# Optimization experiments

Measured on AMD Instinct MI355X. Metric: run time of the kernel, lower is better.

The kernel has to match this reference:

```python
import jax, jax.numpy as jnp
import numpy as np

B, G = 256, 4096
N_GENES, D_GENE = 30000, 256
D_HIDDEN, D_Z = 256, 64
EPS = 1e-8


def setup_inputs() -> dict:
    key = jax.random.key(0)
    ks = jax.random.split(key, 12)
    d_in = D_GENE + 1  # + log-libsize
    s = lambda fan_in: 1.0 / np.sqrt(fan_in)
    return {
        "x": jax.random.uniform(ks[0], (B, G), jnp.float32) * 5.0,  # expression counts
        "gene_indices": jax.random.randint(ks[1], (B, G), 0, N_GENES),
        "emb_table": jax.random.normal(ks[2], (N_GENES, D_GENE), jnp.float32) * 0.02,
        "W1": jax.random.normal(ks[3], (d_in, D_HIDDEN), jnp.float32) * s(d_in),
        "b1": jnp.zeros((D_HIDDEN,), jnp.float32),
        "W2": jax.random.normal(ks[4], (D_HIDDEN, D_HIDDEN), jnp.float32) * s(D_HIDDEN),
        "b2": jnp.zeros((D_HIDDEN,), jnp.float32),
        "Wmu": jax.random.normal(ks[5], (D_HIDDEN, D_Z), jnp.float32) * s(D_HIDDEN),
        "bmu": jnp.zeros((D_Z,), jnp.float32),
        "Wlv": jax.random.normal(ks[6], (D_HIDDEN, D_Z), jnp.float32) * s(D_HIDDEN),
        "blv": jnp.zeros((D_Z,), jnp.float32),
    }


def reference(x, gene_indices, emb_table, W1, b1, W2, b2, Wmu, bmu, Wlv, blv):
    # pool_genes: gather (B,G,d) then weighted-sum reduce to (B,d)
    gene_embs = emb_table[gene_indices]                      # (B, G, d)
    w = jnp.log1p(x)
    w = w / (w.sum(axis=1, keepdims=True) + EPS)             # (B, G)
    h_pool = jnp.einsum('bg,bgd->bd', w, gene_embs)          # (B, d)

    log_lib = jnp.log1p(x.sum(axis=1))[:, None]              # (B, 1)
    h = jnp.concatenate([h_pool, log_lib], axis=-1)          # (B, d+1)

    h = jax.nn.relu(h @ W1 + b1)                             # dropout: eval-mode identity
    h = jax.nn.relu(h @ W2 + b2)
    mu_z = h @ Wmu + bmu
    logvar_z = h @ Wlv + blv
    return (mu_z, logvar_z, h_pool)
```

## Files before the change

kernel.cpp:

```cpp
#include <hip/hip_runtime.h>
#include <math.h>

#define BB      256
#define GG      4096
#define DG      256
#define DH      256
#define DZ      64
#define NGENES  30000
#define KPAD    30016
#define NCHUNK  (KPAD / 32)
#define KSPLIT  128
#define RED     16
#define NPART2  (KSPLIT / RED)
#define HALF    (KPAD / 2)
#define FB_TILES (NCHUNK * 16)
#define SPLIT   4
#define GCHUNK  (GG / SPLIT)

typedef __attribute__((ext_vector_type(8))) short  short8v;
typedef __attribute__((ext_vector_type(4))) float  floatx4;

__device__ __forceinline__ unsigned short bf16_rn(float f) {
    unsigned u = __float_as_uint(f);
    u += 0x7FFFu + ((u >> 16) & 1u);
    return (unsigned short)(u >> 16);
}

__global__ __launch_bounds__(256) void scatter_kernel(
    const float* __restrict__ x,
    const int*   __restrict__ gi,
    unsigned short* __restrict__ W16,
    float* __restrict__ wsum,
    float* __restrict__ xsum)
{
    const int b   = blockIdx.x;
    const int h   = blockIdx.y;
    const int tid = threadIdx.x;
    const int base = h * HALF;

    __shared__ float sW[HALF];
    for (int i = tid; i < HALF; i += 256) sW[i] = 0.f;
    __syncthreads();

    const float4* x4 = (const float4*)(x  + (size_t)b * GG);
    const int4*   g4 = (const int4*)  (gi + (size_t)b * GG);

    float lws = 0.f, xs = 0.f;
    #pragma unroll
    for (int it = 0; it < 4; ++it) {
        const int    e  = it * 256 + tid;
        const float4 xv = x4[e];
        const int4   iv = g4[e];
        const float lw0 = log1pf(xv.x), lw1 = log1pf(xv.y);
        const float lw2 = log1pf(xv.z), lw3 = log1pf(xv.w);
        lws += lw0 + lw1 + lw2 + lw3;
        xs  += xv.x + xv.y + xv.z + xv.w;
        int r0 = iv.x - base, r1 = iv.y - base, r2 = iv.z - base, r3 = iv.w - base;
        if ((unsigned)r0 < (unsigned)HALF) atomicAdd(&sW[r0], lw0);
        if ((unsigned)r1 < (unsigned)HALF) atomicAdd(&sW[r1], lw1);
        if ((unsigned)r2 < (unsigned)HALF) atomicAdd(&sW[r2], lw2);
        if ((unsigned)r3 < (unsigned)HALF) atomicAdd(&sW[r3], lw3);
    }
    __syncthreads();

    uint4* dst = (uint4*)(W16 + (size_t)b * KPAD + base);
    for (int i = tid; i < HALF / 8; i += 256) {
        const float* s = &sW[i * 8];
        uint4 o;
        o.x = (unsigned)bf16_rn(s[0]) | ((unsigned)bf16_rn(s[1]) << 16);
        o.y = (unsigned)bf16_rn(s[2]) | ((unsigned)bf16_rn(s[3]) << 16);
        o.z = (unsigned)bf16_rn(s[4]) | ((unsigned)bf16_rn(s[5]) << 16);
        o.w = (unsigned)bf16_rn(s[6]) | ((unsigned)bf16_rn(s[7]) << 16);
        dst[i] = o;
    }
    __syncthreads();

    #pragma unroll
    for (int off = 32; off > 0; off >>= 1) {
        lws += __shfl_down(lws, off);
        xs  += __shfl_down(xs,  off);
    }
    if ((tid & 63) == 0) { sW[tid >> 6] = lws; sW[4 + (tid >> 6)] = xs; }
    __syncthreads();
    if (tid == 0 && h == 0) {
        wsum[b] = sW[0] + sW[1] + sW[2] + sW[3];
        xsum[b] = sW[4] + sW[5] + sW[6] + sW[7];
    }
}

__global__ __launch_bounds__(256) void fragb_kernel(
    const float* __restrict__ emb, unsigned short* __restrict__ fragB)
{
    const int tile = blockIdx.x * 4 + (threadIdx.x >> 6);
    const int lane = threadIdx.x & 63;
    const int kc = tile >> 4;
    const int nt = tile & 15;
    const int n  = (nt << 4) + (lane & 15);
    const int k0 = (kc << 5) + ((lane >> 4) << 3);

    unsigned short v[8] __attribute__((aligned(16)));
    #pragma unroll
    for (int j = 0; j < 8; ++j) {
        const int k = k0 + j;
        v[j] = (k < NGENES) ? bf16_rn(emb[(size_t)k * DG + n]) : (unsigned short)0;
    }
    *(uint4*)(fragB + (size_t)tile * 512 + lane * 8) = *(const uint4*)v;
}

__global__ __launch_bounds__(256) void gemm_kernel(
    const unsigned short* __restrict__ W16,
    const unsigned short* __restrict__ fragB,
    float* __restrict__ ws_gemm)
{
    const int mt   = blockIdx.x;
    const int ks   = blockIdx.y;
    const int tid  = threadIdx.x;
    const int w    = tid >> 6;
    const int lane = tid & 63;
    const int quad = lane >> 4;
    const int l16  = lane & 15;

    const int q = NCHUNK / KSPLIT;
    const int r = NCHUNK % KSPLIT;
    const int c0  = (ks < r) ? ks * (q + 1) : r * (q + 1) + (ks - r) * q;
    const int cnt = (ks < r) ? (q + 1) : q;

    __shared__ short8v sB[1024];

    const unsigned short* Arow =
        W16 + (size_t)((mt << 6) + (w << 4) + l16) * KPAD + (quad << 3);

    floatx4 acc[16];
    #pragma unroll
    for (int nt = 0; nt < 16; ++nt) acc[nt] = (floatx4){0.f, 0.f, 0.f, 0.f};

    for (int c = 0; c < cnt; ++c) {
        const int kc = c0 + c;

        const short8v af = *(const short8v*)(Arow + (kc << 5));

        const uint4* src = (const uint4*)(fragB + (size_t)kc * 8192);
        #pragma unroll
        for (int i = 0; i < 4; ++i)
            ((uint4*)sB)[i * 256 + tid] = src[i * 256 + tid];

        __syncthreads();
        #pragma unroll
        for (int nt = 0; nt < 16; ++nt) {
            const short8v bf = sB[nt * 64 + lane];
            acc[nt] = __builtin_amdgcn_mfma_f32_16x16x32_bf16(af, bf, acc[nt], 0, 0, 0);
        }
        __syncthreads();
    }

    #pragma unroll
    for (int nt = 0; nt < 16; ++nt) {
        #pragma unroll
        for (int reg = 0; reg < 4; ++reg) {
            const int m = (mt << 6) + (w << 4) + (quad << 2) + reg;
            const int n = (nt << 4) + l16;
            ws_gemm[((size_t)m * KSPLIT + ks) * DG + n] = acc[nt][reg];
        }
    }
}

__global__ __launch_bounds__(256) void reduce_kernel(
    const float* __restrict__ wsg, float* __restrict__ part2)
{
    const int b = blockIdx.x, p = blockIdx.y, d = threadIdx.x;
    const float* src = wsg + ((size_t)b * KSPLIT + p * RED) * DG + d;
    float s = 0.f;
    #pragma unroll
    for (int i = 0; i < RED; ++i) s += src[(size_t)i * DG];
    part2[((size_t)b * NPART2 + p) * DG + d] = s;
}

__global__ __launch_bounds__(256) void convert_kernel(
    const float* __restrict__ emb, unsigned short* __restrict__ embh, int n4)
{
    const float4* e4 = (const float4*)emb;
    ushort4*      o4 = (ushort4*)embh;
    const int stride = gridDim.x * 256;
    for (int i = blockIdx.x * 256 + threadIdx.x; i < n4; i += stride) {
        const float4 v = e4[i];
        ushort4 o;
        o.x = bf16_rn(v.x); o.y = bf16_rn(v.y);
        o.z = bf16_rn(v.z); o.w = bf16_rn(v.w);
        o4[i] = o;
    }
}

__global__ __launch_bounds__(256) void pool_bf16_kernel(
    const float*          __restrict__ x,
    const int*            __restrict__ gi,
    const unsigned short* __restrict__ embh,
    float* __restrict__ ws_pool,
    float* __restrict__ ws_wsum,
    float* __restrict__ ws_xsum)
{
    const int b    = blockIdx.x;
    const int s    = blockIdx.y;
    const int tid  = threadIdx.x;
    const int wave = tid >> 6;
    const int lane = tid & 63;

    const float* xrow = x  + (size_t)b * GG + (size_t)s * GCHUNK;
    const int*   irow = gi + (size_t)b * GG + (size_t)s * GCHUNK;
    const uint2* emb2 = (const uint2*)embh;

    __shared__ float lw_s[256];
    __shared__ int   idx_s[256];
    __shared__ float accred[4][256];
    __shared__ float redw[4], redx[4];

    float wsum = 0.f, xsum = 0.f;
    float4 acc = make_float4(0.f, 0.f, 0.f, 0.f);

    for (int g0 = 0; g0 < GCHUNK; g0 += 256) {
        __syncthreads();
        const float xv = xrow[g0 + tid];
        const int   iv = irow[g0 + tid];
        const float lw = log1pf(xv);
        xsum += xv;
        wsum += lw;
        lw_s[tid]  = lw;
        idx_s[tid] = iv;
        __syncthreads();

        #pragma unroll 8
        for (int k = 0; k < 64; ++k) {
            const int   gidx = (k << 2) | wave;
            const float lw_b = lw_s[gidx];
            const uint2 e    = emb2[(size_t)idx_s[gidx] * 64 + lane];
            acc.x = fmaf(lw_b, __uint_as_float(e.x << 16),         acc.x);
            acc.y = fmaf(lw_b, __uint_as_float(e.x & 0xFFFF0000u), acc.y);
            acc.z = fmaf(lw_b, __uint_as_float(e.y << 16),         acc.z);
            acc.w = fmaf(lw_b, __uint_as_float(e.y & 0xFFFF0000u), acc.w);
        }
    }

    accred[wave][lane * 4 + 0] = acc.x;
    accred[wave][lane * 4 + 1] = acc.y;
    accred[wave][lane * 4 + 2] = acc.z;
    accred[wave][lane * 4 + 3] = acc.w;

    #pragma unroll
    for (int off = 32; off > 0; off >>= 1) {
        wsum += __shfl_down(wsum, off);
        xsum += __shfl_down(xsum, off);
    }
    if (lane == 0) { redw[wave] = wsum; redx[wave] = xsum; }
    __syncthreads();

    const float tot = accred[0][tid] + accred[1][tid] + accred[2][tid] + accred[3][tid];
    ws_pool[((size_t)b * SPLIT + s) * DG + tid] = tot;
    if (tid == 0) {
        ws_wsum[b * SPLIT + s] = redw[0] + redw[1] + redw[2] + redw[3];
        ws_xsum[b * SPLIT + s] = redx[0] + redx[1] + redx[2] + redx[3];
    }
}

template <int NS, int NW>
__global__ __launch_bounds__(512) void mlp_kernel(
    const float* __restrict__ part,
    const float* __restrict__ wsA, const float* __restrict__ xsA,
    const float* __restrict__ W1, const float* __restrict__ b1,
    const float* __restrict__ W2, const float* __restrict__ b2,
    const float* __restrict__ Wmu, const float* __restrict__ bmu,
    const float* __restrict__ Wlv, const float* __restrict__ blv,
    float* __restrict__ out)
{
    const int b   = blockIdx.x;
    const int tid = threadIdx.x;
    const int kq  = tid >> 6;
    const int c4  = tid & 63;

    __shared__ float  h[DH + 1];
    __shared__ float  h1[DH];
    __shared__ float  h2[DH];
    __shared__ float4 red[8][64];
    __shared__ float  redz[8][64];

    if (tid < DH) {
        float acc = 0.f;
        #pragma unroll
        for (int s = 0; s < NS; ++s)
            acc += part[((size_t)b * NS + s) * DG + tid];
        float wsum = 0.f, xsum = 0.f;
        #pragma unroll
        for (int s = 0; s < NW; ++s) {
            wsum += wsA[b * NW + s];
            xsum += xsA[b * NW + s];
        }
        const float hp = acc / (wsum + 1e-8f);
        out[2 * BB * DZ + (size_t)b * DG + tid] = hp;
        h[tid] = hp;
        if (tid == 0) h[DH] = log1pf(xsum);
    }
    __syncthreads();

    {
        const float4* Wv = (const float4*)W1;
        float4 a = make_float4(0.f, 0.f, 0.f, 0.f);
        const int i0 = kq * 32;
        const int i1 = i0 + 32 + (kq == 7 ? 1 : 0);
        for (int i = i0; i < i1; ++i) {
            const float  hi = h[i];
            const float4 w  = Wv[(size_t)i * 64 + c4];
            a.x = fmaf(hi, w.x, a.x);
            a.y = fmaf(hi, w.y, a.y);
            a.z = fmaf(hi, w.z, a.z);
            a.w = fmaf(hi, w.w, a.w);
        }
        red[kq][c4] = a;
        __syncthreads();
        if (tid < 64) {
            float4 t = red[0][tid];
            #pragma unroll
            for (int s = 1; s < 8; ++s) {
                const float4 rr = red[s][tid];
                t.x += rr.x; t.y += rr.y; t.z += rr.z; t.w += rr.w;
            }
            const float4 bb = ((const float4*)b1)[tid];
            h1[4 * tid + 0] = fmaxf(t.x + bb.x, 0.f);
            h1[4 * tid + 1] = fmaxf(t.y + bb.y, 0.f);
            h1[4 * tid + 2] = fmaxf(t.z + bb.z, 0.f);
            h1[4 * tid + 3] = fmaxf(t.w + bb.w, 0.f);
        }
        __syncthreads();
    }

    {
        const float4* Wv = (const float4*)W2;
        float4 a = make_float4(0.f, 0.f, 0.f, 0.f);
        const int i0 = kq * 32;
        for (int i = i0; i < i0 + 32; ++i) {
            const float  hi = h1[i];
            const float4 w  = Wv[(size_t)i * 64 + c4];
            a.x = fmaf(hi, w.x, a.x);
            a.y = fmaf(hi, w.y, a.y);
            a.z = fmaf(hi, w.z, a.z);
            a.w = fmaf(hi, w.w, a.w);
        }
        red[kq][c4] = a;
        __syncthreads();
        if (tid < 64) {
            float4 t = red[0][tid];
            #pragma unroll
            for (int s = 1; s < 8; ++s) {
                const float4 rr = red[s][tid];
                t.x += rr.x; t.y += rr.y; t.z += rr.z; t.w += rr.w;
            }
            const float4 bb = ((const float4*)b2)[tid];
            h2[4 * tid + 0] = fmaxf(t.x + bb.x, 0.f);
            h2[4 * tid + 1] = fmaxf(t.y + bb.y, 0.f);
            h2[4 * tid + 2] = fmaxf(t.z + bb.z, 0.f);
            h2[4 * tid + 3] = fmaxf(t.w + bb.w, 0.f);
        }
        __syncthreads();
    }

    {
        const bool is_lv = tid >= 256;
        const int  j  = tid & 63;
        const int  kh = (tid >> 6) & 3;
        const float* Wz = is_lv ? Wlv : Wmu;
        float az = 0.f;
        for (int i = kh * 64; i < kh * 64 + 64; ++i)
            az = fmaf(h2[i], Wz[(size_t)i * DZ + j], az);
        redz[(is_lv ? 4 : 0) + kh][j] = az;
        __syncthreads();
        if (tid < 2 * DZ) {
            const bool lv = tid >= DZ;
            const int  jj = tid & (DZ - 1);
            const int  base = lv ? 4 : 0;
            float rr = redz[base][jj] + redz[base + 1][jj]
                     + redz[base + 2][jj] + redz[base + 3][jj];
            rr += lv ? blv[jj] : bmu[jj];
            out[(lv ? BB * DZ : 0) + (size_t)b * DZ + jj] = rr;
        }
    }
}

extern "C" void kernel_launch(void* const* d_in, const int* in_sizes, int n_in,
                              void* d_out, int out_size, void* d_ws, size_t ws_size,
                              hipStream_t stream) {
    const float* x    = (const float*)d_in[0];
    const int*   gi   = (const int*)  d_in[1];
    const float* emb  = (const float*)d_in[2];
    const float* W1   = (const float*)d_in[3];
    const float* b1   = (const float*)d_in[4];
    const float* W2   = (const float*)d_in[5];
    const float* b2   = (const float*)d_in[6];
    const float* Wmu  = (const float*)d_in[7];
    const float* bmu  = (const float*)d_in[8];
    const float* Wlv  = (const float*)d_in[9];
    const float* blv  = (const float*)d_in[10];
    float* out = (float*)d_out;

    char* ws = (char*)d_ws;
    float* ws_wsum = (float*)(ws + 0);
    float* ws_xsum = (float*)(ws + 4096);
    const size_t off_main = 8192;

    const size_t szW   = (size_t)BB * KPAD * sizeof(unsigned short);
    const size_t szFB  = (size_t)FB_TILES * 1024;
    const size_t szGP  = (size_t)BB * KSPLIT * DG * sizeof(float);
    const size_t szP2  = (size_t)BB * NPART2 * DG * sizeof(float);
    const size_t need_full = off_main + szW + szFB + szGP + szP2;

    const size_t szPool = (size_t)BB * SPLIT * DG * sizeof(float);
    const size_t szEmbh = (size_t)NGENES * DG * sizeof(unsigned short);
    const size_t need_fb = off_main + szPool + szEmbh;

    if (ws_size >= need_full) {
        unsigned short* Wm    = (unsigned short*)(ws + off_main);
        unsigned short* fragB = (unsigned short*)(ws + off_main + szW);
        float*          wsg   = (float*)(ws + off_main + szW + szFB);
        float*          part2 = (float*)(ws + off_main + szW + szFB + szGP);

        scatter_kernel<<<dim3(BB, 2), 256, 0, stream>>>(x, gi, Wm, ws_wsum, ws_xsum);
        fragb_kernel<<<FB_TILES / 4, 256, 0, stream>>>(emb, fragB);
        gemm_kernel<<<dim3(4, KSPLIT), 256, 0, stream>>>(Wm, fragB, wsg);
        reduce_kernel<<<dim3(BB, NPART2), 256, 0, stream>>>(wsg, part2);
        mlp_kernel<NPART2, 1><<<BB, 512, 0, stream>>>(part2, ws_wsum, ws_xsum,
                                           W1, b1, W2, b2, Wmu, bmu, Wlv, blv, out);
    } else if (ws_size >= need_fb) {
        float*          ws_pool = (float*)(ws + off_main);
        unsigned short* embh    = (unsigned short*)(ws + off_main + szPool);

        convert_kernel<<<2048, 256, 0, stream>>>(emb, embh, NGENES * DG / 4);
        pool_bf16_kernel<<<dim3(BB, SPLIT), 256, 0, stream>>>(
            x, gi, embh, ws_pool, ws_wsum, ws_xsum);
        mlp_kernel<SPLIT, SPLIT><<<BB, 512, 0, stream>>>(ws_pool, ws_wsum, ws_xsum,
                                           W1, b1, W2, b2, Wmu, bmu, Wlv, blv, out);
    }
}
```

Measured before the change: 143.1 us.

## Double-buffer GEMM B tiles and store split-K partials as bf16

The GEMM kernel now prefetches the next K-chunk of B fragments and A into registers while running MFMAs on the current chunk, with a two-slot shared buffer and one barrier per iteration instead of two. The split-K partial sums are rounded to bf16, staged through shared memory, and written as coalesced 16-byte stores, halving the partial-sum workspace traffic. The reduce kernel reads the bf16 partials. This targets load latency and write/read bandwidth of the partial buffer, at the cost of extra precision loss in the split-K partials and more shared memory per block.

Measured after the change: 149.6 us. 4.6% more time.

```diff
diff --git a/kernel.cpp b/kernel.cpp
--- a/kernel.cpp
+++ b/kernel.cpp
@@ -110,7 +110,7 @@
 __global__ __launch_bounds__(256) void gemm_kernel(
     const unsigned short* __restrict__ W16,
     const unsigned short* __restrict__ fragB,
-    float* __restrict__ ws_gemm)
+    unsigned short* __restrict__ wsg16)
 {
     const int mt   = blockIdx.x;
     const int ks   = blockIdx.y;
@@ -122,10 +122,10 @@
 
     const int q = NCHUNK / KSPLIT;
     const int r = NCHUNK % KSPLIT;
-    const int c0  = (ks < r) ? ks * (q + 1) : r * (q + 1) + (ks - r) * q;
-    const int cnt = (ks < r) ? (q + 1) : q;
-
-    __shared__ short8v sB[1024];
+    const int c0  = ks * q + (ks < r ? ks : r);
+    const int cnt = q + (ks < r ? 1 : 0);
+
+    __shared__ short8v sB[2][1024];
 
     const unsigned short* Arow =
         W16 + (size_t)((mt << 6) + (w << 4) + l16) * KPAD + (quad << 3);
@@ -134,44 +134,67 @@
     #pragma unroll
     for (int nt = 0; nt < 16; ++nt) acc[nt] = (floatx4){0.f, 0.f, 0.f, 0.f};
 
+    uint4 breg[4];
+    {
+        const uint4* src = (const uint4*)(fragB + (size_t)c0 * 8192);
+        #pragma unroll
+        for (int i = 0; i < 4; ++i) breg[i] = src[i * 256 + tid];
+    }
+    short8v af = *(const short8v*)(Arow + ((size_t)c0 << 5));
+    #pragma unroll
+    for (int i = 0; i < 4; ++i) ((uint4*)sB[0])[i * 256 + tid] = breg[i];
+    __syncthreads();
+
     for (int c = 0; c < cnt; ++c) {
-        const int kc = c0 + c;
-
-        const short8v af = *(const short8v*)(Arow + (kc << 5));
-
-        const uint4* src = (const uint4*)(fragB + (size_t)kc * 8192);
-        #pragma unroll
-        for (int i = 0; i < 4; ++i)
-            ((uint4*)sB)[i * 256 + tid] = src[i * 256 + tid];
-
-        __syncthreads();
+        const int cur = c & 1;
+        short8v afn;
+        if (c + 1 < cnt) {
+            const uint4* src = (const uint4*)(fragB + (size_t)(c0 + c + 1) * 8192);
+            #pragma unroll
+            for (int i = 0; i < 4; ++i) breg[i] = src[i * 256 + tid];
+            afn = *(const short8v*)(Arow + ((size_t)(c0 + c + 1) << 5));
+        }
         #pragma unroll
         for (int nt = 0; nt < 16; ++nt) {
-            const short8v bf = sB[nt * 64 + lane];
+            const short8v bf = sB[cur][nt * 64 + lane];
             acc[nt] = __builtin_amdgcn_mfma_f32_16x16x32_bf16(af, bf, acc[nt], 0, 0, 0);
         }
-        __syncthreads();
-    }
-
+        if (c + 1 < cnt) {
+            #pragma unroll
+            for (int i = 0; i < 4; ++i) ((uint4*)sB[cur ^ 1])[i * 256 + tid] = breg[i];
+            af = afn;
+        }
+        __syncthreads();
+    }
+
+    unsigned short* epi = (unsigned short*)sB + (w << 12);
     #pragma unroll
     for (int nt = 0; nt < 16; ++nt) {
         #pragma unroll
-        for (int reg = 0; reg < 4; ++reg) {
-            const int m = (mt << 6) + (w << 4) + (quad << 2) + reg;
-            const int n = (nt << 4) + l16;
-            ws_gemm[((size_t)m * KSPLIT + ks) * DG + n] = acc[nt][reg];
-        }
+        for (int reg = 0; reg < 4; ++reg)
+            epi[((quad << 2) + reg) * 256 + (nt << 4) + l16] = bf16_rn(acc[nt][reg]);
+    }
+    uint4* wrow = (uint4*)wsg16;
+    #pragma unroll
+    for (int j = 0; j < 8; ++j) {
+        const int flat = lane + (j << 6);
+        const int rr   = flat >> 5;
+        const int u    = flat & 31;
+        const uint4 v  = *(const uint4*)(epi + rr * 256 + (u << 3));
+        const int m    = (mt << 6) + (w << 4) + rr;
+        wrow[(((size_t)m * KSPLIT + ks) << 5) + u] = v;
     }
 }
 
 __global__ __launch_bounds__(256) void reduce_kernel(
-    const float* __restrict__ wsg, float* __restrict__ part2)
+    const unsigned short* __restrict__ wsg16, float* __restrict__ part2)
 {
     const int b = blockIdx.x, p = blockIdx.y, d = threadIdx.x;
-    const float* src = wsg + ((size_t)b * KSPLIT + p * RED) * DG + d;
+    const unsigned short* src = wsg16 + ((size_t)b * KSPLIT + p * RED) * DG + d;
     float s = 0.f;
     #pragma unroll
-    for (int i = 0; i < RED; ++i) s += src[(size_t)i * DG];
+    for (int i = 0; i < RED; ++i)
+        s += __uint_as_float((unsigned)src[(size_t)i * DG] << 16);
     part2[((size_t)b * NPART2 + p) * DG + d] = s;
 }
 
@@ -405,7 +428,7 @@
 
     const size_t szW   = (size_t)BB * KPAD * sizeof(unsigned short);
     const size_t szFB  = (size_t)FB_TILES * 1024;
-    const size_t szGP  = (size_t)BB * KSPLIT * DG * sizeof(float);
+    const size_t szGP  = (size_t)BB * KSPLIT * DG * sizeof(unsigned short);
     const size_t szP2  = (size_t)BB * NPART2 * DG * sizeof(float);
     const size_t need_full = off_main + szW + szFB + szGP + szP2;
 
@@ -416,13 +439,13 @@
     if (ws_size >= need_full) {
         unsigned short* Wm    = (unsigned short*)(ws + off_main);
         unsigned short* fragB = (unsigned short*)(ws + off_main + szW);
-        float*          wsg   = (float*)(ws + off_main + szW + szFB);
+        unsigned short* wsg16 = (unsigned short*)(ws + off_main + szW + szFB);
         float*          part2 = (float*)(ws + off_main + szW + szFB + szGP);
 
         scatter_kernel<<<dim3(BB, 2), 256, 0, stream>>>(x, gi, Wm, ws_wsum, ws_xsum);
         fragb_kernel<<<FB_TILES / 4, 256, 0, stream>>>(emb, fragB);
-        gemm_kernel<<<dim3(4, KSPLIT), 256, 0, stream>>>(Wm, fragB, wsg);
-        reduce_kernel<<<dim3(BB, NPART2), 256, 0, stream>>>(wsg, part2);
+        gemm_kernel<<<dim3(4, KSPLIT), 256, 0, stream>>>(Wm, fragB, wsg16);
+        reduce_kernel<<<dim3(BB, NPART2), 256, 0, stream>>>(wsg16, part2);
         mlp_kernel<NPART2, 1><<<BB, 512, 0, stream>>>(part2, ws_wsum, ws_xsum,
                                            W1, b1, W2, b2, Wmu, bmu, Wlv, blv, out);
     } else if (ws_size >= need_fb) {
```

## Transpose embeddings via LDS, store split-K partials as bf16, remap gemm blocks

Applied to the files above, without the earlier changes.

fragb_kernel now loads a 32-row chunk of the embedding table with coalesced float4 reads into padded shared memory, then builds the bf16 MFMA B-fragments from LDS. Previously each lane did strided scalar global reads. The gemm kernel writes its split-K partial sums as bf16 instead of fp32, which halves the write and reread traffic through reduce_kernel. It also uses a 1D grid remapped so that blocks sharing the same K-chunk of fragB run close together, which should improve L2 reuse. Rounding the partials to bf16 adds precision loss to the pooled output.

Result: faster. 135.8 us (-5.1%).

```diff
diff --git a/kernel.cpp b/kernel.cpp
--- a/kernel.cpp
+++ b/kernel.cpp
@@ -14,6 +14,7 @@
 #define NPART2  (KSPLIT / RED)
 #define HALF    (KPAD / 2)
 #define FB_TILES (NCHUNK * 16)
+#define TSTRIDE 258
 #define SPLIT   4
 #define GCHUNK  (GG / SPLIT)
 
@@ -91,39 +92,59 @@
 __global__ __launch_bounds__(256) void fragb_kernel(
     const float* __restrict__ emb, unsigned short* __restrict__ fragB)
 {
-    const int tile = blockIdx.x * 4 + (threadIdx.x >> 6);
-    const int lane = threadIdx.x & 63;
-    const int kc = tile >> 4;
-    const int nt = tile & 15;
-    const int n  = (nt << 4) + (lane & 15);
-    const int k0 = (kc << 5) + ((lane >> 4) << 3);
-
-    unsigned short v[8] __attribute__((aligned(16)));
-    #pragma unroll
-    for (int j = 0; j < 8; ++j) {
-        const int k = k0 + j;
-        v[j] = (k < NGENES) ? bf16_rn(emb[(size_t)k * DG + n]) : (unsigned short)0;
-    }
-    *(uint4*)(fragB + (size_t)tile * 512 + lane * 8) = *(const uint4*)v;
-}
-
-__global__ __launch_bounds__(256) void gemm_kernel(
-    const unsigned short* __restrict__ W16,
-    const unsigned short* __restrict__ fragB,
-    float* __restrict__ ws_gemm)
-{
-    const int mt   = blockIdx.x;
-    const int ks   = blockIdx.y;
+    const int kc   = blockIdx.x;
     const int tid  = threadIdx.x;
     const int w    = tid >> 6;
     const int lane = tid & 63;
     const int quad = lane >> 4;
     const int l16  = lane & 15;
+    const int k0   = kc << 5;
+
+    __shared__ float sT[32 * TSTRIDE];
+
+    const float4* e4 = (const float4*)emb;
+    #pragma unroll
+    for (int i = 0; i < 8; ++i) {
+        const int f   = i * 256 + tid;
+        const int row = f >> 6;
+        const int col = f & 63;
+        float4 v = make_float4(0.f, 0.f, 0.f, 0.f);
+        if (k0 + row < NGENES) v = e4[(size_t)(k0 + row) * 64 + col];
+        float* d = &sT[row * TSTRIDE + (col << 2)];
+        *(float2*)d       = make_float2(v.x, v.y);
+        *(float2*)(d + 2) = make_float2(v.z, v.w);
+    }
+    __syncthreads();
+
+    #pragma unroll
+    for (int t = 0; t < 4; ++t) {
+        const int nt = (w << 2) + t;
+        unsigned short v[8] __attribute__((aligned(16)));
+        #pragma unroll
+        for (int j = 0; j < 8; ++j)
+            v[j] = bf16_rn(sT[(quad * 8 + j) * TSTRIDE + (nt << 4) + l16]);
+        *(uint4*)(fragB + (size_t)kc * 8192 + (nt << 9) + lane * 8) = *(const uint4*)v;
+    }
+}
+
+__global__ __launch_bounds__(256) void gemm_kernel(
+    const unsigned short* __restrict__ W16,
+    const unsigned short* __restrict__ fragB,
+    unsigned short* __restrict__ wsg16)
+{
+    const int bid  = blockIdx.x;
+    const int mt   = (bid >> 3) & 3;
+    const int ks   = ((bid >> 5) << 3) | (bid & 7);
+    const int tid  = threadIdx.x;
+    const int w    = tid >> 6;
+    const int lane = tid & 63;
+    const int quad = lane >> 4;
+    const int l16  = lane & 15;
 
     const int q = NCHUNK / KSPLIT;
     const int r = NCHUNK % KSPLIT;
-    const int c0  = (ks < r) ? ks * (q + 1) : r * (q + 1) + (ks - r) * q;
-    const int cnt = (ks < r) ? (q + 1) : q;
+    const int c0  = ks * q + (ks < r ? ks : r);
+    const int cnt = q + (ks < r ? 1 : 0);
 
     __shared__ short8v sB[1024];
 
@@ -137,7 +158,7 @@
     for (int c = 0; c < cnt; ++c) {
         const int kc = c0 + c;
 
-        const short8v af = *(const short8v*)(Arow + (kc << 5));
+        const short8v af = *(const short8v*)(Arow + ((size_t)kc << 5));
 
         const uint4* src = (const uint4*)(fragB + (size_t)kc * 8192);
         #pragma unroll
@@ -159,19 +180,20 @@
         for (int reg = 0; reg < 4; ++reg) {
             const int m = (mt << 6) + (w << 4) + (quad << 2) + reg;
             const int n = (nt << 4) + l16;
-            ws_gemm[((size_t)m * KSPLIT + ks) * DG + n] = acc[nt][reg];
+            wsg16[((size_t)m * KSPLIT + ks) * DG + n] = bf16_rn(acc[nt][reg]);
         }
     }
 }
 
 __global__ __launch_bounds__(256) void reduce_kernel(
-    const float* __restrict__ wsg, float* __restrict__ part2)
+    const unsigned short* __restrict__ wsg16, float* __restrict__ part2)
 {
     const int b = blockIdx.x, p = blockIdx.y, d = threadIdx.x;
-    const float* src = wsg + ((size_t)b * KSPLIT + p * RED) * DG + d;
+    const unsigned short* src = wsg16 + ((size_t)b * KSPLIT + p * RED) * DG + d;
     float s = 0.f;
     #pragma unroll
-    for (int i = 0; i < RED; ++i) s += src[(size_t)i * DG];
+    for (int i = 0; i < RED; ++i)
+        s += __uint_as_float((unsigned)src[(size_t)i * DG] << 16);
     part2[((size_t)b * NPART2 + p) * DG + d] = s;
 }
 
@@ -405,7 +427,7 @@
 
     const size_t szW   = (size_t)BB * KPAD * sizeof(unsigned short);
     const size_t szFB  = (size_t)FB_TILES * 1024;
-    const size_t szGP  = (size_t)BB * KSPLIT * DG * sizeof(float);
+    const size_t szGP  = (size_t)BB * KSPLIT * DG * sizeof(unsigned short);
     const size_t szP2  = (size_t)BB * NPART2 * DG * sizeof(float);
     const size_t need_full = off_main + szW + szFB + szGP + szP2;
 
@@ -416,13 +438,13 @@
     if (ws_size >= need_full) {
         unsigned short* Wm    = (unsigned short*)(ws + off_main);
         unsigned short* fragB = (unsigned short*)(ws + off_main + szW);
-        float*          wsg   = (float*)(ws + off_main + szW + szFB);
+        unsigned short* wsg16 = (unsigned short*)(ws + off_main + szW + szFB);
         float*          part2 = (float*)(ws + off_main + szW + szFB + szGP);
 
         scatter_kernel<<<dim3(BB, 2), 256, 0, stream>>>(x, gi, Wm, ws_wsum, ws_xsum);
-        fragb_kernel<<<FB_TILES / 4, 256, 0, stream>>>(emb, fragB);
-        gemm_kernel<<<dim3(4, KSPLIT), 256, 0, stream>>>(Wm, fragB, wsg);
-        reduce_kernel<<<dim3(BB, NPART2), 256, 0, stream>>>(wsg, part2);
+        fragb_kernel<<<NCHUNK, 256, 0, stream>>>(emb, fragB);
+        gemm_kernel<<<4 * KSPLIT, 256, 0, stream>>>(Wm, fragB, wsg16);
+        reduce_kernel<<<dim3(BB, NPART2), 256, 0, stream>>>(wsg16, part2);
         mlp_kernel<NPART2, 1><<<BB, 512, 0, stream>>>(part2, ws_wsum, ws_xsum,
                                            W1, b1, W2, b2, Wmu, bmu, Wlv, blv, out);
     } else if (ws_size >= need_fb) {
```
